# Kernel tuning notes

Measured on AMD Instinct MI355X. Metric: run time of the kernel, lower is better.

Reference implementation:

```python
import jax, jax.numpy as jnp
import numpy as np


def _lstm_encode(x_tbF, W_ih, W_hh, b_ih, b_hh):
    """torch nn.LSTM (single layer), x: [T, B, F]. Returns final (h, c), each [B, H]."""
    H = W_hh.shape[1]
    B = x_tbF.shape[1]
    b = b_ih + b_hh

    def step(carry, xt):
        h, c = carry
        gates = xt @ W_ih.T + h @ W_hh.T + b  # [B, 4H]
        i, f, g, o = jnp.split(gates, 4, axis=-1)
        c = jax.nn.sigmoid(f) * c + jax.nn.sigmoid(i) * jnp.tanh(g)
        h = jax.nn.sigmoid(o) * jnp.tanh(c)
        return (h, c), None

    init = (jnp.zeros((B, H), x_tbF.dtype), jnp.zeros((B, H), x_tbF.dtype))
    (h, c), _ = jax.lax.scan(step, init, x_tbF)
    return h, c


def reference(speed, pos, Ws_ih, Ws_hh, bs_ih, bs_hh, Wp_ih, Wp_hh, bp_ih, bp_hh,
              Wd_ih, Wd_hh, bd_ih, bd_hh, W_fc, b_fc, W_emb, b_emb, seq_len):
    # Encoders consume time-major inputs (module does speed.permute(1,0,2))
    sh, sc = _lstm_encode(jnp.transpose(speed, (1, 0, 2)), Ws_ih, Ws_hh, bs_ih, bs_hh)
    ph, pc = _lstm_encode(jnp.transpose(pos, (1, 0, 2)), Wp_ih, Wp_hh, bp_ih, bp_hh)

    h0 = ph + sh
    c0 = pc + sc
    last_pos0 = pos[:, -1, :]  # [B, 4]
    bd = bd_ih + bd_hh

    def dec_step(carry, _):
        h, c, last_pos = carry
        gates = last_pos @ Wd_ih.T + h @ Wd_hh.T + bd  # [B, 4H]
        i, f, g, o = jnp.split(gates, 4, axis=-1)
        c = jax.nn.sigmoid(f) * c + jax.nn.sigmoid(i) * jnp.tanh(g)
        h = jax.nn.sigmoid(o) * jnp.tanh(c)
        crossing = jax.nn.relu(h @ W_fc.T + b_fc)        # fc_crossing: [B, 2]
        last_pos = jax.nn.relu(crossing @ W_emb.T + b_emb)  # pos_embedding: [B, 4]
        probs = jax.nn.softmax(crossing, axis=1)
        return (h, c, last_pos), probs

    _, probs = jax.lax.scan(dec_step, (h0, c0, last_pos0), None, length=seq_len)
    return jnp.transpose(probs, (1, 0, 2))  # [B, seq_len, 2]


def setup_inputs() -> dict:
    B, T, H, F = 8192, 16, 512, 4
    seq_len = 16
    key = jax.random.key(0)
    ks = jax.random.split(key, 20)
    s = 1.0 / np.sqrt(H)

    def u(k, shape):
        return jax.random.uniform(k, shape, jnp.float32, -s, s)

    return {
        "speed": jax.random.normal(ks[0], (B, T, F), jnp.float32),
        "pos": jax.random.normal(ks[1], (B, T, F), jnp.float32),
        "Ws_ih": u(ks[2], (4 * H, F)), "Ws_hh": u(ks[3], (4 * H, H)),
        "bs_ih": u(ks[4], (4 * H,)), "bs_hh": u(ks[5], (4 * H,)),
        "Wp_ih": u(ks[6], (4 * H, F)), "Wp_hh": u(ks[7], (4 * H, H)),
        "bp_ih": u(ks[8], (4 * H,)), "bp_hh": u(ks[9], (4 * H,)),
        "Wd_ih": u(ks[10], (4 * H, F)), "Wd_hh": u(ks[11], (4 * H, H)),
        "bd_ih": u(ks[12], (4 * H,)), "bd_hh": u(ks[13], (4 * H,)),
        "W_fc": u(ks[14], (2, H)), "b_fc": u(ks[15], (2,)),
        "W_emb": u(ks[16], (4, 2)), "b_emb": u(ks[17], (4,)),
        "seq_len": seq_len,
    }
```

## Files before the change

kernel.cpp:

```cpp
#include <hip/hip_runtime.h>

#define NBLK 256
#define NTHR 512
#define MTILE 32
#define KPADI 592
#define HSTR  528
#define CHB   (9*8*64*16)
#define LSTR  (16*CHB)

typedef __attribute__((ext_vector_type(4))) int int4v;

__device__ inline float ex2(float x){ return __builtin_amdgcn_exp2f(x); }
__device__ inline float rcpf_(float d){ return __builtin_amdgcn_rcpf(d); }
__device__ inline float rcpn(float d){ float r=__builtin_amdgcn_rcpf(d); return r*(2.f-d*r); }
#define LOG2E 1.4426950408889634f
__device__ inline float sigf(float x){ return rcpf_(1.f+ex2(-LOG2E*x)); }
__device__ inline float tanh_(float x){ return 2.f*rcpf_(1.f+ex2(-2.f*LOG2E*x))-1.f; }

__global__ void scale_k(const float* Ws_ih, const float* Ws_hh, const float* bs_ih, const float* bs_hh,
                        const float* Wp_ih, const float* Wp_hh, const float* bp_ih, const float* bp_hh,
                        const float* Wd_ih, const float* Wd_hh, const float* bd_ih, const float* bd_hh,
                        int* smax)
{
    int L = blockIdx.x >> 5;
    int blk = blockIdx.x & 31;
    const float* Wih = L==0 ? Ws_ih : L==1 ? Wp_ih : Wd_ih;
    const float* Whh = L==0 ? Ws_hh : L==1 ? Wp_hh : Wd_hh;
    const float* bih = L==0 ? bs_ih : L==1 ? bp_ih : bd_ih;
    const float* bhh = L==0 ? bs_hh : L==1 ? bp_hh : bd_hh;
    float m = 0.f;
    for (int i = blk*256 + threadIdx.x; i < 2048*512; i += 32*256) m = fmaxf(m, fabsf(Whh[i]));
    for (int i = blk*256 + threadIdx.x; i < 2048*4;   i += 32*256) m = fmaxf(m, fabsf(Wih[i]));
    for (int i = blk*256 + threadIdx.x; i < 2048;     i += 32*256) m = fmaxf(m, 0.5f*fabsf(bih[i]+bhh[i]));
    __shared__ float red[256];
    red[threadIdx.x] = m; __syncthreads();
    for (int s = 128; s; s >>= 1){
        if (threadIdx.x < s) red[threadIdx.x] = fmaxf(red[threadIdx.x], red[threadIdx.x+s]);
        __syncthreads();
    }
    if (threadIdx.x == 0) atomicMax(&smax[L], __float_as_int(red[0]));
}

__global__ void pack_k(const float* Wih, const float* Whh, const float* bih, const float* bhh,
                       const int* smax, int L, unsigned char* dst, float* gsout)
{
    int f4 = blockIdx.x*256 + threadIdx.x;
    if (f4*4 >= LSTR) return;
    float mx = __int_as_float(smax[L]);
    float inv = 127.f / mx;
    if (blockIdx.x==0 && threadIdx.x==0) gsout[L] = mx * (1.f/(127.f*127.f));
    int fb = f4*4;
    int lane=(fb>>4)&63, nt=(fb>>10)&7, t=fb>>13;
    int kt=t%9, chunk=t/9;
    int n = (chunk*8+nt)*16 + (lane&15);
    int ch=n>>7, g=(n>>5)&3, u=n&31;
    int row = g*512 + ch*32 + u;
    int kbase = kt*64 + ((lane>>4)<<4) + (fb&15);
    unsigned out = 0;
    #pragma unroll
    for (int b=0;b<4;++b){
        int k = kbase + b;
        float v = 0.f;
        if (k < 512)      v = Whh[row*512+k];
        else if (k < 528) v = Wih[row*4 + (k&3)];
        else if (k < 530) v = 0.5f*(bih[row]+bhh[row]);
        int q = (int)rintf(v*inv);
        q = q>127?127:(q<-127?-127:q);
        out |= ((unsigned)(q & 255)) << (8*b);
    }
    *(unsigned*)(dst + fb) = out;
}

__global__ __launch_bounds__(NTHR, 1)
void lstm_all(const float* __restrict__ speed, const float* __restrict__ pos,
              const unsigned char* __restrict__ wpack, const float* __restrict__ gsb,
              const float* __restrict__ wfc, const float* __restrict__ bfc,
              const float* __restrict__ wemb, const float* __restrict__ bemb,
              float* __restrict__ out)
{
    __shared__ __align__(16) unsigned char abuf[2][MTILE][KPADI];
    __shared__ __align__(16) unsigned char hsave[MTILE][HSTR];
    __shared__ float csave[MTILE][512];
    __shared__ float smallw[1040];
    __shared__ float partial[NTHR];

    const int tid  = threadIdx.x;
    const int lane = tid & 63;
    const int wv   = tid >> 6;
    const int row0 = blockIdx.x * MTILE;
    const int l15  = lane & 15;
    const int lq   = lane >> 4;
    const int cstag = blockIdx.x & 15;

    const float gs0 = gsb[0], gs1 = gsb[1], gs2 = gsb[2];

    {
        for (int i = tid; i < 2*MTILE*(KPADI/16); i += NTHR) {
            int b = i / (MTILE*(KPADI/16));
            int rmd = i % (MTILE*(KPADI/16));
            int m = rmd / (KPADI/16), c16 = (rmd % (KPADI/16))*16;
            *(int4v*)&abuf[b][m][c16] = (int4v){0,0,0,0};
        }
        for (int i = tid; i < 1024; i += NTHR) smallw[i] = wfc[i];
        if (tid < 2) smallw[1024+tid] = bfc[tid];
        if (tid < 8) smallw[1026+tid] = wemb[tid];
        if (tid < 4) smallw[1034+tid] = bemb[tid];
    }
    __syncthreads();
    if (tid < 64) { int b = tid>>5, m = tid&31; abuf[b][m][528] = 127; abuf[b][m][529] = 127; }
    if (tid < 128) {
        int m = tid>>2, f3 = tid&3;
        float x = speed[((size_t)(row0+m)*16 + 0)*4 + f3];
        int q = (int)rintf(fminf(fmaxf(x*31.75f,-127.f),127.f));
        unsigned char qb = (unsigned char)q;
        abuf[0][m][512+f3]=qb; abuf[0][m][516+f3]=qb; abuf[0][m][520+f3]=qb; abuf[0][m][524+f3]=qb;
    }
    __syncthreads();

    float cc0[16], cc1[16];
    #pragma unroll
    for (int i = 0; i < 16; ++i) { cc0[i]=0.f; cc1[i]=0.f; }

    int4v bA[8], bB[8];

    auto epi = [&](int4v (&acc)[2][8], float (&cc)[16], int chunk, int wbuf,
                   float nK1, float nK2){
        #pragma unroll
        for (int mf=0;mf<2;++mf)
            #pragma unroll
            for (int up=0;up<2;++up)
                #pragma unroll
                for (int r=0;r<4;++r){
                    int idx = (mf*2+up)*4 + r;
                    float fi = (float)acc[mf][0+up][r];
                    float ff = (float)acc[mf][2+up][r];
                    float fg = (float)acc[mf][4+up][r];
                    float fo = (float)acc[mf][6+up][r];
                    float si = rcpf_(1.f+ex2(nK1*fi));
                    float sf = rcpf_(1.f+ex2(nK1*ff));
                    float so = rcpf_(1.f+ex2(nK1*fo));
                    float tg = 2.f*rcpf_(1.f+ex2(nK2*fg)) - 1.f;
                    float cn = sf*cc[idx] + si*tg;
                    cc[idx] = cn;
                    float h = so*tanh_(cn);
                    int q = (int)rintf(h*127.f);
                    abuf[wbuf][mf*16+lq*4+r][chunk*32+up*16+l15] = (unsigned char)q;
                }
    };

    auto step2 = [&](int rb, int wbuf, const unsigned char* wl,
                     float (&c0)[16], float (&c1)[16], float gs, int WARM, int PF){
        const int ch0 = (2*wv + 0 + cstag) & 15;
        const int ch1 = (2*wv + 1 + cstag) & 15;
        const unsigned char* bp0 = wl + (size_t)ch0*CHB + lane*16;
        const unsigned char* bp1 = wl + (size_t)ch1*CHB + lane*16;
        const unsigned char* ar0 = &abuf[rb][l15][0];
        const unsigned char* ar1 = &abuf[rb][16+l15][0];
        const float nK1 = -gs*LOG2E, nK2 = -2.f*gs*LOG2E;
        int4v acc[2][8];
        if (!WARM){
            #pragma unroll
            for (int nt=0;nt<8;++nt) bA[nt] = *(const int4v*)(bp0 + nt*1024);
        }
        #pragma unroll
        for (int mf=0;mf<2;++mf)
            #pragma unroll
            for (int nt=0;nt<8;++nt) acc[mf][nt] = (int4v){0,0,0,0};
        #pragma unroll 1
        for (int kt=0; kt<8; kt+=2){
            const unsigned char* p1 = bp0 + (kt+1)*8192;
            #pragma unroll
            for (int nt=0;nt<8;++nt) bB[nt] = *(const int4v*)(p1 + nt*1024);
            int4v a0 = *(const int4v*)(ar0 + kt*64 + lq*16);
            int4v a1 = *(const int4v*)(ar1 + kt*64 + lq*16);
            #pragma unroll
            for (int nt=0;nt<8;++nt){
                acc[0][nt] = __builtin_amdgcn_mfma_i32_16x16x64_i8(a0, bA[nt], acc[0][nt], 0,0,0);
                acc[1][nt] = __builtin_amdgcn_mfma_i32_16x16x64_i8(a1, bA[nt], acc[1][nt], 0,0,0);
            }
            const unsigned char* p2 = bp0 + (kt+2)*8192;
            #pragma unroll
            for (int nt=0;nt<8;++nt) bA[nt] = *(const int4v*)(p2 + nt*1024);
            a0 = *(const int4v*)(ar0 + (kt+1)*64 + lq*16);
            a1 = *(const int4v*)(ar1 + (kt+1)*64 + lq*16);
            #pragma unroll
            for (int nt=0;nt<8;++nt){
                acc[0][nt] = __builtin_amdgcn_mfma_i32_16x16x64_i8(a0, bB[nt], acc[0][nt], 0,0,0);
                acc[1][nt] = __builtin_amdgcn_mfma_i32_16x16x64_i8(a1, bB[nt], acc[1][nt], 0,0,0);
            }
        }
        #pragma unroll
        for (int nt=0;nt<8;++nt) bB[nt] = *(const int4v*)(bp1 + nt*1024);
        {
            int4v a0 = *(const int4v*)(ar0 + 8*64 + lq*16);
            int4v a1 = *(const int4v*)(ar1 + 8*64 + lq*16);
            #pragma unroll
            for (int nt=0;nt<8;++nt){
                acc[0][nt] = __builtin_amdgcn_mfma_i32_16x16x64_i8(a0, bA[nt], acc[0][nt], 0,0,0);
                acc[1][nt] = __builtin_amdgcn_mfma_i32_16x16x64_i8(a1, bA[nt], acc[1][nt], 0,0,0);
            }
        }
        epi(acc, c0, ch0, wbuf, nK1, nK2);
        #pragma unroll
        for (int mf=0;mf<2;++mf)
            #pragma unroll
            for (int nt=0;nt<8;++nt) acc[mf][nt] = (int4v){0,0,0,0};
        #pragma unroll 1
        for (int kt=0; kt<8; kt+=2){
            const unsigned char* p1 = bp1 + (kt+1)*8192;
            #pragma unroll
            for (int nt=0;nt<8;++nt) bA[nt] = *(const int4v*)(p1 + nt*1024);
            int4v a0 = *(const int4v*)(ar0 + kt*64 + lq*16);
            int4v a1 = *(const int4v*)(ar1 + kt*64 + lq*16);
            #pragma unroll
            for (int nt=0;nt<8;++nt){
                acc[0][nt] = __builtin_amdgcn_mfma_i32_16x16x64_i8(a0, bB[nt], acc[0][nt], 0,0,0);
                acc[1][nt] = __builtin_amdgcn_mfma_i32_16x16x64_i8(a1, bB[nt], acc[1][nt], 0,0,0);
            }
            const unsigned char* p2 = bp1 + (kt+2)*8192;
            #pragma unroll
            for (int nt=0;nt<8;++nt) bB[nt] = *(const int4v*)(p2 + nt*1024);
            a0 = *(const int4v*)(ar0 + (kt+1)*64 + lq*16);
            a1 = *(const int4v*)(ar1 + (kt+1)*64 + lq*16);
            #pragma unroll
            for (int nt=0;nt<8;++nt){
                acc[0][nt] = __builtin_amdgcn_mfma_i32_16x16x64_i8(a0, bA[nt], acc[0][nt], 0,0,0);
                acc[1][nt] = __builtin_amdgcn_mfma_i32_16x16x64_i8(a1, bA[nt], acc[1][nt], 0,0,0);
            }
        }
        if (PF){
            #pragma unroll
            for (int nt=0;nt<8;++nt) bA[nt] = *(const int4v*)(bp0 + nt*1024);
        }
        {
            int4v a0 = *(const int4v*)(ar0 + 8*64 + lq*16);
            int4v a1 = *(const int4v*)(ar1 + 8*64 + lq*16);
            #pragma unroll
            for (int nt=0;nt<8;++nt){
                acc[0][nt] = __builtin_amdgcn_mfma_i32_16x16x64_i8(a0, bB[nt], acc[0][nt], 0,0,0);
                acc[1][nt] = __builtin_amdgcn_mfma_i32_16x16x64_i8(a1, bB[nt], acc[1][nt], 0,0,0);
            }
        }
        epi(acc, c1, ch1, wbuf, nK1, nK2);
    };

    auto pass_dual = [&](const unsigned char* wl, int s, float (&cc)[16], float gs, int (&hq)[16]) {
        const int chunk = (2*wv + s + cstag) & 15;
        const unsigned char* bp = wl + (size_t)chunk*CHB + lane*16;
        const unsigned char* ar0 = &abuf[0][l15][0];
        const unsigned char* ar1 = &abuf[0][16+l15][0];
        int4v acc[2][8];
        #pragma unroll
        for (int mf=0;mf<2;++mf)
            #pragma unroll
            for (int nt=0;nt<8;++nt) acc[mf][nt] = (int4v){0,0,0,0};
        #pragma unroll
        for (int nt=0;nt<8;++nt) bA[nt] = *(const int4v*)(bp + nt*1024);
        #pragma unroll 1
        for (int kt=0; kt<8; kt+=2){
            const unsigned char* p1 = bp + (kt+1)*8192;
            #pragma unroll
            for (int nt=0;nt<8;++nt) bB[nt] = *(const int4v*)(p1 + nt*1024);
            int4v a0 = *(const int4v*)(ar0 + kt*64 + lq*16);
            int4v a1 = *(const int4v*)(ar1 + kt*64 + lq*16);
            #pragma unroll
            for (int nt=0;nt<8;++nt){
                acc[0][nt] = __builtin_amdgcn_mfma_i32_16x16x64_i8(a0, bA[nt], acc[0][nt], 0,0,0);
                acc[1][nt] = __builtin_amdgcn_mfma_i32_16x16x64_i8(a1, bA[nt], acc[1][nt], 0,0,0);
            }
            const unsigned char* p2 = bp + (kt+2)*8192;
            #pragma unroll
            for (int nt=0;nt<8;++nt) bA[nt] = *(const int4v*)(p2 + nt*1024);
            a0 = *(const int4v*)(ar0 + (kt+1)*64 + lq*16);
            a1 = *(const int4v*)(ar1 + (kt+1)*64 + lq*16);
            #pragma unroll
            for (int nt=0;nt<8;++nt){
                acc[0][nt] = __builtin_amdgcn_mfma_i32_16x16x64_i8(a0, bB[nt], acc[0][nt], 0,0,0);
                acc[1][nt] = __builtin_amdgcn_mfma_i32_16x16x64_i8(a1, bB[nt], acc[1][nt], 0,0,0);
            }
        }
        {
            int4v a0 = *(const int4v*)(ar0 + 8*64 + lq*16);
            int4v a1 = *(const int4v*)(ar1 + 8*64 + lq*16);
            #pragma unroll
            for (int nt=0;nt<8;++nt){
                acc[0][nt] = __builtin_amdgcn_mfma_i32_16x16x64_i8(a0, bA[nt], acc[0][nt], 0,0,0);
                acc[1][nt] = __builtin_amdgcn_mfma_i32_16x16x64_i8(a1, bA[nt], acc[1][nt], 0,0,0);
            }
        }
        {
            const unsigned char* hr0 = &hsave[l15][0];
            const unsigned char* hr1 = &hsave[16+l15][0];
            #pragma unroll
            for (int nt=0;nt<8;++nt) bA[nt] = *(const int4v*)(bp + nt*1024);
            #pragma unroll 1
            for (int kt=0; kt<8; kt+=2){
                const unsigned char* p1 = bp + (kt+1)*8192;
                #pragma unroll
                for (int nt=0;nt<8;++nt) bB[nt] = *(const int4v*)(p1 + nt*1024);
                int4v a0 = *(const int4v*)(hr0 + kt*64 + lq*16);
                int4v a1 = *(const int4v*)(hr1 + kt*64 + lq*16);
                #pragma unroll
                for (int nt=0;nt<8;++nt){
                    acc[0][nt] = __builtin_amdgcn_mfma_i32_16x16x64_i8(a0, bA[nt], acc[0][nt], 0,0,0);
                    acc[1][nt] = __builtin_amdgcn_mfma_i32_16x16x64_i8(a1, bA[nt], acc[1][nt], 0,0,0);
                }
                const unsigned char* p2 = bp + (kt+2)*8192;
                #pragma unroll
                for (int nt=0;nt<8;++nt) bA[nt] = *(const int4v*)(p2 + nt*1024);
                a0 = *(const int4v*)(hr0 + (kt+1)*64 + lq*16);
                a1 = *(const int4v*)(hr1 + (kt+1)*64 + lq*16);
                #pragma unroll
                for (int nt=0;nt<8;++nt){
                    acc[0][nt] = __builtin_amdgcn_mfma_i32_16x16x64_i8(a0, bB[nt], acc[0][nt], 0,0,0);
                    acc[1][nt] = __builtin_amdgcn_mfma_i32_16x16x64_i8(a1, bB[nt], acc[1][nt], 0,0,0);
                }
            }
        }
        #pragma unroll
        for (int mf=0;mf<2;++mf)
            #pragma unroll
            for (int up=0;up<2;++up)
                #pragma unroll
                for (int r=0;r<4;++r){
                    int idx = (mf*2+up)*4 + r;
                    float gi = (float)acc[mf][0+up][r] * gs;
                    float gf = (float)acc[mf][2+up][r] * gs;
                    float gg = (float)acc[mf][4+up][r] * gs;
                    float go = (float)acc[mf][6+up][r] * gs;
                    float cn = sigf(gf)*cc[idx] + sigf(gi)*tanh_(gg);
                    cc[idx] = cn;
                    float h = sigf(go)*tanh_(cn);
                    hq[idx] = (int)rintf(h*127.f);
                }
    };

    const unsigned char* wsp = wpack;
    const unsigned char* wpp = wpack + (size_t)LSTR;
    const unsigned char* wdp = wpack + 2*(size_t)LSTR;

    #pragma unroll 1
    for (int t=0;t<16;++t){
        int rb=t&1, wbuf=(t+1)&1;
        if (t<15 && tid<128){
            int m=tid>>2, f3=tid&3;
            float x = speed[((size_t)(row0+m)*16 + t+1)*4 + f3];
            int q = (int)rintf(fminf(fmaxf(x*31.75f,-127.f),127.f));
            unsigned char qb=(unsigned char)q;
            abuf[wbuf][m][512+f3]=qb; abuf[wbuf][m][516+f3]=qb; abuf[wbuf][m][520+f3]=qb; abuf[wbuf][m][524+f3]=qb;
        }
        step2(rb,wbuf,wsp,cc0,cc1,gs0, (t>0), (t<15));
        __syncthreads();
    }
    for (int i=tid; i<MTILE*32; i+=NTHR){
        int m=i>>5, cb=(i&31)*16;
        *(int4v*)&hsave[m][cb] = *(const int4v*)&abuf[0][m][cb];
        *(int4v*)&abuf[0][m][cb] = (int4v){0,0,0,0};
    }
    #pragma unroll
    for (int s2=0;s2<2;++s2)
        #pragma unroll
        for (int mf=0;mf<2;++mf)
            #pragma unroll
            for (int up=0;up<2;++up)
                #pragma unroll
                for (int r=0;r<4;++r){
                    int idx=(mf*2+up)*4+r;
                    int ch=(2*wv+s2+cstag)&15;
                    csave[mf*16+lq*4+r][ch*32+up*16+l15] = s2 ? cc1[idx] : cc0[idx];
                }
    #pragma unroll
    for (int i=0;i<16;++i){ cc0[i]=0.f; cc1[i]=0.f; }
    if (tid < 128) {
        int m = tid>>2, f3 = tid&3;
        float x = pos[((size_t)(row0+m)*16 + 0)*4 + f3];
        int q = (int)rintf(fminf(fmaxf(x*31.75f,-127.f),127.f));
        unsigned char qb = (unsigned char)q;
        abuf[0][m][512+f3]=qb; abuf[0][m][516+f3]=qb; abuf[0][m][520+f3]=qb; abuf[0][m][524+f3]=qb;
    }
    __syncthreads();

    #pragma unroll 1
    for (int t=0;t<16;++t){
        int rb=t&1, wbuf=(t+1)&1;
        if (t<15 && tid<128){
            int m=tid>>2, f3=tid&3;
            float x = pos[((size_t)(row0+m)*16 + t+1)*4 + f3];
            int q = (int)rintf(fminf(fmaxf(x*31.75f,-127.f),127.f));
            unsigned char qb=(unsigned char)q;
            abuf[wbuf][m][512+f3]=qb; abuf[wbuf][m][516+f3]=qb; abuf[wbuf][m][520+f3]=qb; abuf[wbuf][m][524+f3]=qb;
        }
        step2(rb,wbuf,wpp,cc0,cc1,gs1, (t>0), (t<15));
        __syncthreads();
    }
    if (tid < 128) {
        int m = tid>>2, f3 = tid&3;
        float x = pos[((size_t)(row0+m)*16 + 15)*4 + f3];
        int q = (int)rintf(fminf(fmaxf(x*31.75f,-127.f),127.f));
        unsigned char qb = (unsigned char)q;
        abuf[0][m][512+f3]=qb; abuf[0][m][516+f3]=qb; abuf[0][m][520+f3]=qb; abuf[0][m][524+f3]=qb;
    }
    #pragma unroll
    for (int s2=0;s2<2;++s2)
        #pragma unroll
        for (int mf=0;mf<2;++mf)
            #pragma unroll
            for (int up=0;up<2;++up)
                #pragma unroll
                for (int r=0;r<4;++r){
                    int idx=(mf*2+up)*4+r;
                    int ch=(2*wv+s2+cstag)&15;
                    float v = csave[mf*16+lq*4+r][ch*32+up*16+l15];
                    if (s2) cc1[idx]+=v; else cc0[idx]+=v;
                }
    __syncthreads();

    #pragma unroll 1
    for (int t=0;t<16;++t){
        int hb;
        if (t == 0) {
            int hq0[16], hq1[16];
            pass_dual(wdp, 0, cc0, gs2, hq0);
            pass_dual(wdp, 1, cc1, gs2, hq1);
            __syncthreads();
            #pragma unroll
            for (int s2=0;s2<2;++s2)
                #pragma unroll
                for (int mf=0;mf<2;++mf)
                    #pragma unroll
                    for (int up=0;up<2;++up)
                        #pragma unroll
                        for (int r=0;r<4;++r){
                            int idx=(mf*2+up)*4+r;
                            int ch=(2*wv+s2+cstag)&15;
                            int q = s2 ? hq1[idx] : hq0[idx];
                            abuf[0][mf*16+lq*4+r][ch*32+up*16+l15] = (unsigned char)q;
                        }
            hb = 0;
        } else {
            int rb=(t+1)&1, wbuf=t&1;
            step2(rb,wbuf,wdp,cc0,cc1,gs2, (t>1), (t<15));
            hb = wbuf;
        }
        __syncthreads();
        {
            int r = lane>>1, col = lane&1;
            const unsigned char* hp = &abuf[hb][r][wv*64];
            const float* wp = &smallw[col*512 + wv*64];
            float p = 0.f;
            #pragma unroll
            for (int k4=0;k4<16;++k4){
                int v = *(const int*)(hp + k4*4);
                p += (float)((signed char)(v    )) * wp[k4*4+0];
                p += (float)((signed char)(v>>8 )) * wp[k4*4+1];
                p += (float)((signed char)(v>>16)) * wp[k4*4+2];
                p += (float)((signed char)(v>>24)) * wp[k4*4+3];
            }
            partial[wv*64 + lane] = p;
        }
        __syncthreads();
        if (wv == 0) {
            float p = 0.f;
            #pragma unroll
            for (int i=0;i<8;++i) p += partial[i*64 + lane];
            int r = lane>>1, col = lane&1;
            p = p*(1.f/127.f) + smallw[1024+col];
            float cr = fmaxf(p, 0.f);
            float other = __shfl_xor(cr, 1, 64);
            float mx = fmaxf(cr, other);
            float e0 = ex2(LOG2E*(cr-mx)), e1 = ex2(LOG2E*(other-mx));
            out[((size_t)(row0+r))*32 + t*2 + col] = e0*rcpn(e0+e1);
            float c0v = col ? other : cr;
            float c1v = col ? cr : other;
            #pragma unroll
            for (int q2=0;q2<2;++q2){
                int e = col*2 + q2;
                float lp = fmaxf(c0v*smallw[1026+e*2] + c1v*smallw[1026+e*2+1] + smallw[1034+e], 0.f);
                int qv = (int)rintf(fminf(lp*31.75f, 127.f));
                unsigned char qb = (unsigned char)qv;
                abuf[hb][r][512+e]=qb; abuf[hb][r][516+e]=qb; abuf[hb][r][520+e]=qb; abuf[hb][r][524+e]=qb;
            }
        }
        __syncthreads();
    }
}

extern "C" void kernel_launch(void* const* d_in, const int* in_sizes, int n_in,
                              void* d_out, int out_size, void* d_ws, size_t ws_size,
                              hipStream_t stream)
{
    (void)in_sizes; (void)n_in; (void)out_size; (void)ws_size;
    const float* speed = (const float*)d_in[0];
    const float* pos   = (const float*)d_in[1];
    const float* Ws_ih = (const float*)d_in[2];
    const float* Ws_hh = (const float*)d_in[3];
    const float* bs_ih = (const float*)d_in[4];
    const float* bs_hh = (const float*)d_in[5];
    const float* Wp_ih = (const float*)d_in[6];
    const float* Wp_hh = (const float*)d_in[7];
    const float* bp_ih = (const float*)d_in[8];
    const float* bp_hh = (const float*)d_in[9];
    const float* Wd_ih = (const float*)d_in[10];
    const float* Wd_hh = (const float*)d_in[11];
    const float* bd_ih = (const float*)d_in[12];
    const float* bd_hh = (const float*)d_in[13];
    const float* W_fc  = (const float*)d_in[14];
    const float* b_fc  = (const float*)d_in[15];
    const float* W_emb = (const float*)d_in[16];
    const float* b_emb = (const float*)d_in[17];

    unsigned char* wp8 = (unsigned char*)d_ws;
    int*   smax  = (int*)(wp8 + 3*(size_t)LSTR);
    float* gsout = (float*)(wp8 + 3*(size_t)LSTR + 16);

    scale_k<<<96, 256, 0, stream>>>(Ws_ih,Ws_hh,bs_ih,bs_hh, Wp_ih,Wp_hh,bp_ih,bp_hh,
                                    Wd_ih,Wd_hh,bd_ih,bd_hh, smax);
    int gb = (LSTR/4 + 255) / 256;
    pack_k<<<gb, 256, 0, stream>>>(Ws_ih, Ws_hh, bs_ih, bs_hh, smax, 0, wp8,                  gsout);
    pack_k<<<gb, 256, 0, stream>>>(Wp_ih, Wp_hh, bp_ih, bp_hh, smax, 1, wp8 +   (size_t)LSTR, gsout);
    pack_k<<<gb, 256, 0, stream>>>(Wd_ih, Wd_hh, bd_ih, bd_hh, smax, 2, wp8 + 2*(size_t)LSTR, gsout);
    lstm_all<<<NBLK, NTHR, 0, stream>>>(speed, pos, wp8, gsout,
                                        W_fc, b_fc, W_emb, b_emb, (float*)d_out);
}
```

Measured before the change: 726.6 us.

## Deepen weight-fragment prefetch across passes and use LDS-only barriers

Restructures the int8 MFMA LSTM step so both B-fragment register sets (bA/bB) are kept two k-tiles ahead. Each pass also prefetches the first two tiles of the next chunk, including across layer boundaries, so global weight loads overlap the MFMA work and the activation epilogue. __syncthreads is replaced with an inline-asm barrier that waits only on LDS counters, which lets outstanding global prefetches stay in flight across barriers. The costs are higher register pressure and an inline-asm barrier that leans on the compiler to insert the vmcnt waits before the prefetched registers are used.

```diff
diff --git a/kernel.cpp b/kernel.cpp
--- a/kernel.cpp
+++ b/kernel.cpp
@@ -16,6 +16,10 @@
 #define LOG2E 1.4426950408889634f
 __device__ inline float sigf(float x){ return rcpf_(1.f+ex2(-LOG2E*x)); }
 __device__ inline float tanh_(float x){ return 2.f*rcpf_(1.f+ex2(-2.f*LOG2E*x))-1.f; }
+
+__device__ inline void lbar(){
+    asm volatile("s_waitcnt lgkmcnt(0)\n\ts_barrier" ::: "memory");
+}
 
 __global__ void scale_k(const float* Ws_ih, const float* Ws_hh, const float* bs_ih, const float* bs_hh,
                         const float* Wp_ih, const float* Wp_hh, const float* bp_ih, const float* bp_hh,
@@ -94,6 +98,24 @@
 
     const float gs0 = gsb[0], gs1 = gsb[1], gs2 = gsb[2];
 
+    const int ch0 = (2*wv + 0 + cstag) & 15;
+    const int ch1 = (2*wv + 1 + cstag) & 15;
+    const unsigned char* wsp = wpack;
+    const unsigned char* wpp = wpack + (size_t)LSTR;
+    const unsigned char* wdp = wpack + 2*(size_t)LSTR;
+    const unsigned char* sp0 = wsp + (size_t)ch0*CHB + lane*16;
+    const unsigned char* sp1 = wsp + (size_t)ch1*CHB + lane*16;
+    const unsigned char* pp0 = wpp + (size_t)ch0*CHB + lane*16;
+    const unsigned char* pp1 = wpp + (size_t)ch1*CHB + lane*16;
+    const unsigned char* dp0 = wdp + (size_t)ch0*CHB + lane*16;
+    const unsigned char* dp1 = wdp + (size_t)ch1*CHB + lane*16;
+
+    int4v bA[8], bB[8];
+    #pragma unroll
+    for (int nt=0;nt<8;++nt) bA[nt] = *(const int4v*)(sp0 + nt*1024);
+    #pragma unroll
+    for (int nt=0;nt<8;++nt) bB[nt] = *(const int4v*)(sp0 + 8192 + nt*1024);
+
     {
         for (int i = tid; i < 2*MTILE*(KPADI/16); i += NTHR) {
             int b = i / (MTILE*(KPADI/16));
@@ -106,7 +128,7 @@
         if (tid < 8) smallw[1026+tid] = wemb[tid];
         if (tid < 4) smallw[1034+tid] = bemb[tid];
     }
-    __syncthreads();
+    lbar();
     if (tid < 64) { int b = tid>>5, m = tid&31; abuf[b][m][528] = 127; abuf[b][m][529] = 127; }
     if (tid < 128) {
         int m = tid>>2, f3 = tid&3;
@@ -115,13 +137,11 @@
         unsigned char qb = (unsigned char)q;
         abuf[0][m][512+f3]=qb; abuf[0][m][516+f3]=qb; abuf[0][m][520+f3]=qb; abuf[0][m][524+f3]=qb;
     }
-    __syncthreads();
+    lbar();
 
     float cc0[16], cc1[16];
     #pragma unroll
     for (int i = 0; i < 16; ++i) { cc0[i]=0.f; cc1[i]=0.f; }
-
-    int4v bA[8], bB[8];
 
     auto epi = [&](int4v (&acc)[2][8], float (&cc)[16], int chunk, int wbuf,
                    float nK1, float nK2){
@@ -148,105 +168,81 @@
                 }
     };
 
-    auto step2 = [&](int rb, int wbuf, const unsigned char* wl,
-                     float (&c0)[16], float (&c1)[16], float gs, int WARM, int PF){
-        const int ch0 = (2*wv + 0 + cstag) & 15;
-        const int ch1 = (2*wv + 1 + cstag) & 15;
-        const unsigned char* bp0 = wl + (size_t)ch0*CHB + lane*16;
-        const unsigned char* bp1 = wl + (size_t)ch1*CHB + lane*16;
+    auto pass = [&](int rb, int wbuf, const unsigned char* bp, const unsigned char* bpn,
+                    float (&cc)[16], int chunk, float nK1, float nK2,
+                    int4v (&bT)[8], int4v (&bU)[8]){
         const unsigned char* ar0 = &abuf[rb][l15][0];
         const unsigned char* ar1 = &abuf[rb][16+l15][0];
-        const float nK1 = -gs*LOG2E, nK2 = -2.f*gs*LOG2E;
         int4v acc[2][8];
-        if (!WARM){
-            #pragma unroll
-            for (int nt=0;nt<8;++nt) bA[nt] = *(const int4v*)(bp0 + nt*1024);
-        }
         #pragma unroll
         for (int mf=0;mf<2;++mf)
             #pragma unroll
             for (int nt=0;nt<8;++nt) acc[mf][nt] = (int4v){0,0,0,0};
         #pragma unroll 1
-        for (int kt=0; kt<8; kt+=2){
-            const unsigned char* p1 = bp0 + (kt+1)*8192;
-            #pragma unroll
-            for (int nt=0;nt<8;++nt) bB[nt] = *(const int4v*)(p1 + nt*1024);
+        for (int kt=0; kt<6; kt+=2){
             int4v a0 = *(const int4v*)(ar0 + kt*64 + lq*16);
             int4v a1 = *(const int4v*)(ar1 + kt*64 + lq*16);
             #pragma unroll
             for (int nt=0;nt<8;++nt){
-                acc[0][nt] = __builtin_amdgcn_mfma_i32_16x16x64_i8(a0, bA[nt], acc[0][nt], 0,0,0);
-                acc[1][nt] = __builtin_amdgcn_mfma_i32_16x16x64_i8(a1, bA[nt], acc[1][nt], 0,0,0);
-            }
-            const unsigned char* p2 = bp0 + (kt+2)*8192;
-            #pragma unroll
-            for (int nt=0;nt<8;++nt) bA[nt] = *(const int4v*)(p2 + nt*1024);
+                acc[0][nt] = __builtin_amdgcn_mfma_i32_16x16x64_i8(a0, bT[nt], acc[0][nt], 0,0,0);
+                acc[1][nt] = __builtin_amdgcn_mfma_i32_16x16x64_i8(a1, bT[nt], acc[1][nt], 0,0,0);
+            }
+            const unsigned char* p2 = bp + (kt+2)*8192;
+            #pragma unroll
+            for (int nt=0;nt<8;++nt) bT[nt] = *(const int4v*)(p2 + nt*1024);
             a0 = *(const int4v*)(ar0 + (kt+1)*64 + lq*16);
             a1 = *(const int4v*)(ar1 + (kt+1)*64 + lq*16);
             #pragma unroll
             for (int nt=0;nt<8;++nt){
-                acc[0][nt] = __builtin_amdgcn_mfma_i32_16x16x64_i8(a0, bB[nt], acc[0][nt], 0,0,0);
-                acc[1][nt] = __builtin_amdgcn_mfma_i32_16x16x64_i8(a1, bB[nt], acc[1][nt], 0,0,0);
-            }
-        }
-        #pragma unroll
-        for (int nt=0;nt<8;++nt) bB[nt] = *(const int4v*)(bp1 + nt*1024);
+                acc[0][nt] = __builtin_amdgcn_mfma_i32_16x16x64_i8(a0, bU[nt], acc[0][nt], 0,0,0);
+                acc[1][nt] = __builtin_amdgcn_mfma_i32_16x16x64_i8(a1, bU[nt], acc[1][nt], 0,0,0);
+            }
+            const unsigned char* p3 = bp + (kt+3)*8192;
+            #pragma unroll
+            for (int nt=0;nt<8;++nt) bU[nt] = *(const int4v*)(p3 + nt*1024);
+        }
+        {
+            int4v a0 = *(const int4v*)(ar0 + 6*64 + lq*16);
+            int4v a1 = *(const int4v*)(ar1 + 6*64 + lq*16);
+            #pragma unroll
+            for (int nt=0;nt<8;++nt){
+                acc[0][nt] = __builtin_amdgcn_mfma_i32_16x16x64_i8(a0, bT[nt], acc[0][nt], 0,0,0);
+                acc[1][nt] = __builtin_amdgcn_mfma_i32_16x16x64_i8(a1, bT[nt], acc[1][nt], 0,0,0);
+            }
+            if (lane < 32){
+                const unsigned char* p8 = bp + 8*8192;
+                #pragma unroll
+                for (int nt=0;nt<8;++nt) bT[nt] = *(const int4v*)(p8 + nt*1024);
+            }
+        }
+        {
+            int4v a0 = *(const int4v*)(ar0 + 7*64 + lq*16);
+            int4v a1 = *(const int4v*)(ar1 + 7*64 + lq*16);
+            #pragma unroll
+            for (int nt=0;nt<8;++nt){
+                acc[0][nt] = __builtin_amdgcn_mfma_i32_16x16x64_i8(a0, bU[nt], acc[0][nt], 0,0,0);
+                acc[1][nt] = __builtin_amdgcn_mfma_i32_16x16x64_i8(a1, bU[nt], acc[1][nt], 0,0,0);
+            }
+            #pragma unroll
+            for (int nt=0;nt<8;++nt) bU[nt] = *(const int4v*)(bpn + nt*1024);
+        }
         {
             int4v a0 = *(const int4v*)(ar0 + 8*64 + lq*16);
             int4v a1 = *(const int4v*)(ar1 + 8*64 + lq*16);
             #pragma unroll
             for (int nt=0;nt<8;++nt){
-                acc[0][nt] = __builtin_amdgcn_mfma_i32_16x16x64_i8(a0, bA[nt], acc[0][nt], 0,0,0);
-                acc[1][nt] = __builtin_amdgcn_mfma_i32_16x16x64_i8(a1, bA[nt], acc[1][nt], 0,0,0);
-            }
-        }
-        epi(acc, c0, ch0, wbuf, nK1, nK2);
-        #pragma unroll
-        for (int mf=0;mf<2;++mf)
-            #pragma unroll
-            for (int nt=0;nt<8;++nt) acc[mf][nt] = (int4v){0,0,0,0};
-        #pragma unroll 1
-        for (int kt=0; kt<8; kt+=2){
-            const unsigned char* p1 = bp1 + (kt+1)*8192;
-            #pragma unroll
-            for (int nt=0;nt<8;++nt) bA[nt] = *(const int4v*)(p1 + nt*1024);
-            int4v a0 = *(const int4v*)(ar0 + kt*64 + lq*16);
-            int4v a1 = *(const int4v*)(ar1 + kt*64 + lq*16);
-            #pragma unroll
-            for (int nt=0;nt<8;++nt){
-                acc[0][nt] = __builtin_amdgcn_mfma_i32_16x16x64_i8(a0, bB[nt], acc[0][nt], 0,0,0);
-                acc[1][nt] = __builtin_amdgcn_mfma_i32_16x16x64_i8(a1, bB[nt], acc[1][nt], 0,0,0);
-            }
-            const unsigned char* p2 = bp1 + (kt+2)*8192;
-            #pragma unroll
-            for (int nt=0;nt<8;++nt) bB[nt] = *(const int4v*)(p2 + nt*1024);
-            a0 = *(const int4v*)(ar0 + (kt+1)*64 + lq*16);
-            a1 = *(const int4v*)(ar1 + (kt+1)*64 + lq*16);
-            #pragma unroll
-            for (int nt=0;nt<8;++nt){
-                acc[0][nt] = __builtin_amdgcn_mfma_i32_16x16x64_i8(a0, bA[nt], acc[0][nt], 0,0,0);
-                acc[1][nt] = __builtin_amdgcn_mfma_i32_16x16x64_i8(a1, bA[nt], acc[1][nt], 0,0,0);
-            }
-        }
-        if (PF){
-            #pragma unroll
-            for (int nt=0;nt<8;++nt) bA[nt] = *(const int4v*)(bp0 + nt*1024);
-        }
-        {
-            int4v a0 = *(const int4v*)(ar0 + 8*64 + lq*16);
-            int4v a1 = *(const int4v*)(ar1 + 8*64 + lq*16);
-            #pragma unroll
-            for (int nt=0;nt<8;++nt){
-                acc[0][nt] = __builtin_amdgcn_mfma_i32_16x16x64_i8(a0, bB[nt], acc[0][nt], 0,0,0);
-                acc[1][nt] = __builtin_amdgcn_mfma_i32_16x16x64_i8(a1, bB[nt], acc[1][nt], 0,0,0);
-            }
-        }
-        epi(acc, c1, ch1, wbuf, nK1, nK2);
+                acc[0][nt] = __builtin_amdgcn_mfma_i32_16x16x64_i8(a0, bT[nt], acc[0][nt], 0,0,0);
+                acc[1][nt] = __builtin_amdgcn_mfma_i32_16x16x64_i8(a1, bT[nt], acc[1][nt], 0,0,0);
+            }
+            #pragma unroll
+            for (int nt=0;nt<8;++nt) bT[nt] = *(const int4v*)(bpn + 8192 + nt*1024);
+        }
+        epi(acc, cc, chunk, wbuf, nK1, nK2);
     };
 
-    auto pass_dual = [&](const unsigned char* wl, int s, float (&cc)[16], float gs, int (&hq)[16]) {
-        const int chunk = (2*wv + s + cstag) & 15;
-        const unsigned char* bp = wl + (size_t)chunk*CHB + lane*16;
+    auto pass_dual = [&](const unsigned char* bp, const unsigned char* bpn,
+                         float (&cc)[16], float gs, int (&hq)[16],
+                         int4v (&bT)[8], int4v (&bU)[8]){
         const unsigned char* ar0 = &abuf[0][l15][0];
         const unsigned char* ar1 = &abuf[0][16+l15][0];
         int4v acc[2][8];
@@ -254,67 +250,112 @@
         for (int mf=0;mf<2;++mf)
             #pragma unroll
             for (int nt=0;nt<8;++nt) acc[mf][nt] = (int4v){0,0,0,0};
-        #pragma unroll
-        for (int nt=0;nt<8;++nt) bA[nt] = *(const int4v*)(bp + nt*1024);
         #pragma unroll 1
-        for (int kt=0; kt<8; kt+=2){
-            const unsigned char* p1 = bp + (kt+1)*8192;
-            #pragma unroll
-            for (int nt=0;nt<8;++nt) bB[nt] = *(const int4v*)(p1 + nt*1024);
+        for (int kt=0; kt<6; kt+=2){
             int4v a0 = *(const int4v*)(ar0 + kt*64 + lq*16);
             int4v a1 = *(const int4v*)(ar1 + kt*64 + lq*16);
             #pragma unroll
             for (int nt=0;nt<8;++nt){
-                acc[0][nt] = __builtin_amdgcn_mfma_i32_16x16x64_i8(a0, bA[nt], acc[0][nt], 0,0,0);
-                acc[1][nt] = __builtin_amdgcn_mfma_i32_16x16x64_i8(a1, bA[nt], acc[1][nt], 0,0,0);
+                acc[0][nt] = __builtin_amdgcn_mfma_i32_16x16x64_i8(a0, bT[nt], acc[0][nt], 0,0,0);
+                acc[1][nt] = __builtin_amdgcn_mfma_i32_16x16x64_i8(a1, bT[nt], acc[1][nt], 0,0,0);
             }
             const unsigned char* p2 = bp + (kt+2)*8192;
             #pragma unroll
-            for (int nt=0;nt<8;++nt) bA[nt] = *(const int4v*)(p2 + nt*1024);
+            for (int nt=0;nt<8;++nt) bT[nt] = *(const int4v*)(p2 + nt*1024);
             a0 = *(const int4v*)(ar0 + (kt+1)*64 + lq*16);
             a1 = *(const int4v*)(ar1 + (kt+1)*64 + lq*16);
             #pragma unroll
             for (int nt=0;nt<8;++nt){
-                acc[0][nt] = __builtin_amdgcn_mfma_i32_16x16x64_i8(a0, bB[nt], acc[0][nt], 0,0,0);
-                acc[1][nt] = __builtin_amdgcn_mfma_i32_16x16x64_i8(a1, bB[nt], acc[1][nt], 0,0,0);
-            }
+                acc[0][nt] = __builtin_amdgcn_mfma_i32_16x16x64_i8(a0, bU[nt], acc[0][nt], 0,0,0);
+                acc[1][nt] = __builtin_amdgcn_mfma_i32_16x16x64_i8(a1, bU[nt], acc[1][nt], 0,0,0);
+            }
+            const unsigned char* p3 = bp + (kt+3)*8192;
+            #pragma unroll
+            for (int nt=0;nt<8;++nt) bU[nt] = *(const int4v*)(p3 + nt*1024);
+        }
+        {
+            int4v a0 = *(const int4v*)(ar0 + 6*64 + lq*16);
+            int4v a1 = *(const int4v*)(ar1 + 6*64 + lq*16);
+            #pragma unroll
+            for (int nt=0;nt<8;++nt){
+                acc[0][nt] = __builtin_amdgcn_mfma_i32_16x16x64_i8(a0, bT[nt], acc[0][nt], 0,0,0);
+                acc[1][nt] = __builtin_amdgcn_mfma_i32_16x16x64_i8(a1, bT[nt], acc[1][nt], 0,0,0);
+            }
+            if (lane < 32){
+                const unsigned char* p8 = bp + 8*8192;
+                #pragma unroll
+                for (int nt=0;nt<8;++nt) bT[nt] = *(const int4v*)(p8 + nt*1024);
+            }
+        }
+        {
+            int4v a0 = *(const int4v*)(ar0 + 7*64 + lq*16);
+            int4v a1 = *(const int4v*)(ar1 + 7*64 + lq*16);
+            #pragma unroll
+            for (int nt=0;nt<8;++nt){
+                acc[0][nt] = __builtin_amdgcn_mfma_i32_16x16x64_i8(a0, bU[nt], acc[0][nt], 0,0,0);
+                acc[1][nt] = __builtin_amdgcn_mfma_i32_16x16x64_i8(a1, bU[nt], acc[1][nt], 0,0,0);
+            }
+            #pragma unroll
+            for (int nt=0;nt<8;++nt) bU[nt] = *(const int4v*)(bp + nt*1024);
         }
         {
             int4v a0 = *(const int4v*)(ar0 + 8*64 + lq*16);
             int4v a1 = *(const int4v*)(ar1 + 8*64 + lq*16);
             #pragma unroll
             for (int nt=0;nt<8;++nt){
-                acc[0][nt] = __builtin_amdgcn_mfma_i32_16x16x64_i8(a0, bA[nt], acc[0][nt], 0,0,0);
-                acc[1][nt] = __builtin_amdgcn_mfma_i32_16x16x64_i8(a1, bA[nt], acc[1][nt], 0,0,0);
-            }
+                acc[0][nt] = __builtin_amdgcn_mfma_i32_16x16x64_i8(a0, bT[nt], acc[0][nt], 0,0,0);
+                acc[1][nt] = __builtin_amdgcn_mfma_i32_16x16x64_i8(a1, bT[nt], acc[1][nt], 0,0,0);
+            }
+            #pragma unroll
+            for (int nt=0;nt<8;++nt) bT[nt] = *(const int4v*)(bp + 8192 + nt*1024);
         }
         {
             const unsigned char* hr0 = &hsave[l15][0];
             const unsigned char* hr1 = &hsave[16+l15][0];
-            #pragma unroll
-            for (int nt=0;nt<8;++nt) bA[nt] = *(const int4v*)(bp + nt*1024);
             #pragma unroll 1
-            for (int kt=0; kt<8; kt+=2){
-                const unsigned char* p1 = bp + (kt+1)*8192;
-                #pragma unroll
-                for (int nt=0;nt<8;++nt) bB[nt] = *(const int4v*)(p1 + nt*1024);
+            for (int kt=0; kt<6; kt+=2){
                 int4v a0 = *(const int4v*)(hr0 + kt*64 + lq*16);
                 int4v a1 = *(const int4v*)(hr1 + kt*64 + lq*16);
                 #pragma unroll
                 for (int nt=0;nt<8;++nt){
-                    acc[0][nt] = __builtin_amdgcn_mfma_i32_16x16x64_i8(a0, bA[nt], acc[0][nt], 0,0,0);
-                    acc[1][nt] = __builtin_amdgcn_mfma_i32_16x16x64_i8(a1, bA[nt], acc[1][nt], 0,0,0);
+                    acc[0][nt] = __builtin_amdgcn_mfma_i32_16x16x64_i8(a0, bU[nt], acc[0][nt], 0,0,0);
+                    acc[1][nt] = __builtin_amdgcn_mfma_i32_16x16x64_i8(a1, bU[nt], acc[1][nt], 0,0,0);
                 }
                 const unsigned char* p2 = bp + (kt+2)*8192;
                 #pragma unroll
-                for (int nt=0;nt<8;++nt) bA[nt] = *(const int4v*)(p2 + nt*1024);
+                for (int nt=0;nt<8;++nt) bU[nt] = *(const int4v*)(p2 + nt*1024);
                 a0 = *(const int4v*)(hr0 + (kt+1)*64 + lq*16);
                 a1 = *(const int4v*)(hr1 + (kt+1)*64 + lq*16);
                 #pragma unroll
                 for (int nt=0;nt<8;++nt){
-                    acc[0][nt] = __builtin_amdgcn_mfma_i32_16x16x64_i8(a0, bB[nt], acc[0][nt], 0,0,0);
-                    acc[1][nt] = __builtin_amdgcn_mfma_i32_16x16x64_i8(a1, bB[nt], acc[1][nt], 0,0,0);
-                }
+                    acc[0][nt] = __builtin_amdgcn_mfma_i32_16x16x64_i8(a0, bT[nt], acc[0][nt], 0,0,0);
+                    acc[1][nt] = __builtin_amdgcn_mfma_i32_16x16x64_i8(a1, bT[nt], acc[1][nt], 0,0,0);
+                }
+                const unsigned char* p3 = bp + (kt+3)*8192;
+                #pragma unroll
+                for (int nt=0;nt<8;++nt) bT[nt] = *(const int4v*)(p3 + nt*1024);
+            }
+            {
+                int4v a0 = *(const int4v*)(hr0 + 6*64 + lq*16);
+                int4v a1 = *(const int4v*)(hr1 + 6*64 + lq*16);
+                #pragma unroll
+                for (int nt=0;nt<8;++nt){
+                    acc[0][nt] = __builtin_amdgcn_mfma_i32_16x16x64_i8(a0, bU[nt], acc[0][nt], 0,0,0);
+                    acc[1][nt] = __builtin_amdgcn_mfma_i32_16x16x64_i8(a1, bU[nt], acc[1][nt], 0,0,0);
+                }
+                #pragma unroll
+                for (int nt=0;nt<8;++nt) bU[nt] = *(const int4v*)(bpn + nt*1024);
+            }
+            {
+                int4v a0 = *(const int4v*)(hr0 + 7*64 + lq*16);
+                int4v a1 = *(const int4v*)(hr1 + 7*64 + lq*16);
+                #pragma unroll
+                for (int nt=0;nt<8;++nt){
+                    acc[0][nt] = __builtin_amdgcn_mfma_i32_16x16x64_i8(a0, bT[nt], acc[0][nt], 0,0,0);
+                    acc[1][nt] = __builtin_amdgcn_mfma_i32_16x16x64_i8(a1, bT[nt], acc[1][nt], 0,0,0);
+                }
+                #pragma unroll
+                for (int nt=0;nt<8;++nt) bT[nt] = *(const int4v*)(bpn + 8192 + nt*1024);
             }
         }
         #pragma unroll
@@ -335,10 +376,7 @@
                 }
     };
 
-    const unsigned char* wsp = wpack;
-    const unsigned char* wpp = wpack + (size_t)LSTR;
-    const unsigned char* wdp = wpack + 2*(size_t)LSTR;
-
+    const float nK1s = -gs0*LOG2E, nK2s = -2.f*gs0*LOG2E;
     #pragma unroll 1
     for (int t=0;t<16;++t){
         int rb=t&1, wbuf=(t+1)&1;
@@ -349,8 +387,9 @@
             unsigned char qb=(unsigned char)q;
             abuf[wbuf][m][512+f3]=qb; abuf[wbuf][m][516+f3]=qb; abuf[wbuf][m][520+f3]=qb; abuf[wbuf][m][524+f3]=qb;
         }
-        step2(rb,wbuf,wsp,cc0,cc1,gs0, (t>0), (t<15));
-        __syncthreads();
+        pass(rb,wbuf, sp0, sp1,                cc0, ch0, nK1s,nK2s, bA,bB);
+        pass(rb,wbuf, sp1, (t<15)? sp0 : pp0,  cc1, ch1, nK1s,nK2s, bB,bA);
+        lbar();
     }
     for (int i=tid; i<MTILE*32; i+=NTHR){
         int m=i>>5, cb=(i&31)*16;
@@ -378,8 +417,9 @@
         unsigned char qb = (unsigned char)q;
         abuf[0][m][512+f3]=qb; abuf[0][m][516+f3]=qb; abuf[0][m][520+f3]=qb; abuf[0][m][524+f3]=qb;
     }
-    __syncthreads();
-
+    lbar();
+
+    const float nK1p = -gs1*LOG2E, nK2p = -2.f*gs1*LOG2E;
     #pragma unroll 1
     for (int t=0;t<16;++t){
         int rb=t&1, wbuf=(t+1)&1;
@@ -390,8 +430,9 @@
             unsigned char qb=(unsigned char)q;
             abuf[wbuf][m][512+f3]=qb; abuf[wbuf][m][516+f3]=qb; abuf[wbuf][m][520+f3]=qb; abuf[wbuf][m][524+f3]=qb;
         }
-        step2(rb,wbuf,wpp,cc0,cc1,gs1, (t>0), (t<15));
-        __syncthreads();
+        pass(rb,wbuf, pp0, pp1,                cc0, ch0, nK1p,nK2p, bA,bB);
+        pass(rb,wbuf, pp1, (t<15)? pp0 : dp0,  cc1, ch1, nK1p,nK2p, bB,bA);
+        lbar();
     }
     if (tid < 128) {
         int m = tid>>2, f3 = tid&3;
@@ -413,16 +454,17 @@
                     float v = csave[mf*16+lq*4+r][ch*32+up*16+l15];
                     if (s2) cc1[idx]+=v; else cc0[idx]+=v;
                 }
-    __syncthreads();
-
+    lbar();
+
+    const float nK1d = -gs2*LOG2E, nK2d = -2.f*gs2*LOG2E;
     #pragma unroll 1
     for (int t=0;t<16;++t){
         int hb;
         if (t == 0) {
             int hq0[16], hq1[16];
-            pass_dual(wdp, 0, cc0, gs2, hq0);
-            pass_dual(wdp, 1, cc1, gs2, hq1);
-            __syncthreads();
+            pass_dual(dp0, dp1, cc0, gs2, hq0, bA,bB);
+            pass_dual(dp1, dp0, cc1, gs2, hq1, bB,bA);
+            lbar();
             #pragma unroll
             for (int s2=0;s2<2;++s2)
                 #pragma unroll
@@ -439,10 +481,11 @@
             hb = 0;
         } else {
             int rb=(t+1)&1, wbuf=t&1;
-            step2(rb,wbuf,wdp,cc0,cc1,gs2, (t>1), (t<15));
+            pass(rb,wbuf, dp0, dp1, cc0, ch0, nK1d,nK2d, bA,bB);
+            pass(rb,wbuf, dp1, dp0, cc1, ch1, nK1d,nK2d, bB,bA);
             hb = wbuf;
         }
-        __syncthreads();
+        lbar();
         {
             int r = lane>>1, col = lane&1;
             const unsigned char* hp = &abuf[hb][r][wv*64];
@@ -458,7 +501,7 @@
             }
             partial[wv*64 + lane] = p;
         }
-        __syncthreads();
+        lbar();
         if (wv == 0) {
             float p = 0.f;
             #pragma unroll
@@ -481,7 +524,7 @@
                 abuf[hb][r][512+e]=qb; abuf[hb][r][516+e]=qb; abuf[hb][r][520+e]=qb; abuf[hb][r][524+e]=qb;
             }
         }
-        __syncthreads();
+        lbar();
     }
 }
 
```

Result: slower. 1.178 ms, median of 2 (+62.1%).
